# Performance work log

Measured on AMD Instinct MI355X. Metric: run time of the kernel, lower is better.

## Reference

```python
import jax, jax.numpy as jnp
import numpy as np
from jax import lax

B, L, DIM = 2, 2048, 2048
HK, HV = 16, 32
DK, DV = 128, 128
KCONV = 4
KEY_DIM = HK * DK          # 2048
VAL_DIM = HV * DV          # 4096
CONV_DIM = 2 * KEY_DIM + VAL_DIM  # 8192
EPS = 1e-6


def _l2norm(x, eps=1e-6):
    return x * lax.rsqrt((x * x).sum(-1, keepdims=True) + eps)


def _gated_delta_rule(q, k, v, g, beta):
    # q,k: (B,L,H,DK); v: (B,L,H,DV); g,beta: (B,L,H)
    q = _l2norm(q.astype(jnp.float32)) * (DK ** -0.5)
    k = _l2norm(k.astype(jnp.float32))
    v = v.astype(jnp.float32)
    g = g.astype(jnp.float32)
    beta = beta.astype(jnp.float32)
    # time-major for scan: (L,B,H,...)
    qs = q.transpose(1, 0, 2, 3)
    ks = k.transpose(1, 0, 2, 3)
    vs = v.transpose(1, 0, 2, 3)
    gs = g.transpose(1, 0, 2)
    bs = beta.transpose(1, 0, 2)
    state0 = jnp.zeros((B, HV, DK, DV), jnp.float32)

    def step(state, inp):
        q_t, k_t, v_t, g_t, b_t = inp
        state = state * jnp.exp(g_t)[..., None, None]          # decay
        kv_mem = jnp.einsum('bhk,bhkv->bhv', k_t, state)       # read
        delta = (v_t - kv_mem) * b_t[..., None]                # error-correct
        state = state + jnp.einsum('bhk,bhv->bhkv', k_t, delta)
        out_t = jnp.einsum('bhk,bhkv->bhv', q_t, state)
        return state, out_t

    _, outs = lax.scan(step, state0, (qs, ks, vs, gs, bs))
    return outs.transpose(1, 0, 2, 3)  # (B,L,H,DV)


def setup_inputs() -> dict:
    key = jax.random.key(0)
    ks = jax.random.split(key, 8)
    s = 0.02
    return {
        'x': jax.random.normal(ks[0], (B, L, DIM), jnp.float32),
        'W_qkv': jax.random.normal(ks[1], (CONV_DIM, DIM), jnp.float32) * s,
        'W_z': jax.random.normal(ks[2], (VAL_DIM, DIM), jnp.float32) * s,
        'W_a': jax.random.normal(ks[3], (HV, DIM), jnp.float32) * s,
        'W_b': jax.random.normal(ks[4], (HV, DIM), jnp.float32) * s,
        'conv_w': jax.random.normal(ks[5], (CONV_DIM, 1, KCONV), jnp.float32) * 0.2,
        'A_log': jnp.log(jax.random.uniform(ks[6], (HV,), jnp.float32, 1e-6, 16.0)),
        'dt_bias': jnp.ones((HV,), jnp.float32),
        'norm_weight': jnp.ones((DV,), jnp.float32),
        'W_out': jax.random.normal(ks[7], (DIM, VAL_DIM), jnp.float32) * s,
    }


def reference(x, W_qkv, W_z, W_a, W_b, conv_w, A_log, dt_bias, norm_weight, W_out):
    qkv = x @ W_qkv.T                      # (B,L,CONV_DIM)
    z = x @ W_z.T                          # (B,L,VAL_DIM)
    a = x @ W_a.T                          # (B,L,HV)
    b = x @ W_b.T                          # (B,L,HV)
    # depthwise causal conv1d (left pad K-1)
    h = qkv.transpose(0, 2, 1)             # (B,C,L)
    h = lax.conv_general_dilated(h, conv_w, window_strides=(1,),
                                 padding=[(KCONV - 1, 0)],
                                 dimension_numbers=('NCH', 'OIH', 'NCH'),
                                 feature_group_count=CONV_DIM)
    qkv = jax.nn.silu(h.transpose(0, 2, 1))
    q, k, v = jnp.split(qkv, [KEY_DIM, 2 * KEY_DIM], axis=-1)
    q = q.reshape(B, L, HK, DK)
    k = k.reshape(B, L, HK, DK)
    v = v.reshape(B, L, HV, DV)
    rep = HV // HK
    if rep > 1:
        q = jnp.repeat(q, rep, axis=2)
        k = jnp.repeat(k, rep, axis=2)
    g = -jnp.exp(A_log.astype(jnp.float32)) * jax.nn.softplus(a.astype(jnp.float32) + dt_bias)
    beta = jax.nn.sigmoid(b)
    out = _gated_delta_rule(q, k, v, g, beta)   # (B,L,HV,DV) fp32
    # gated RMSNorm over DV: silu(z) * weight * norm(out)
    var = (out * out).mean(-1, keepdims=True)
    out = out * lax.rsqrt(var + EPS) * norm_weight
    zg = z.reshape(B, L, HV, DV)
    out = out * jax.nn.silu(zg.astype(jnp.float32))
    out = out.astype(x.dtype).reshape(B, L, VAL_DIM)
    return out @ W_out.T
```

## Files before the change

### kernel.cpp

```cpp
#include <hip/hip_runtime.h>
#include <hip/hip_bf16.h>
#include <cstddef>
#include <cstdint>

constexpr int B = 2, L = 2048, DIM = 2048;
constexpr int HK = 16, HV = 32, DK = 128, DV = 128;
constexpr int KEY_DIM = HK * DK;
constexpr int VAL_DIM = HV * DV;
constexpr int CONV_DIM = 2 * KEY_DIM + VAL_DIM;
constexpr int NPROJ = CONV_DIM + VAL_DIM + HV + HV;
constexpr int NPAD  = ((NPROJ + 255) / 256) * 256;
constexpr size_t ROWS = (size_t)B * L;
constexpr float EPS = 1e-6f;
constexpr int CHUNK = 64, NCHUNK = L / CHUNK;
constexpr int NCH_TOT = B * HV * NCHUNK;
constexpr int CONV_LT = 16;
constexpr int CONV_TL = L / CONV_LT;

constexpr size_t OFF_QKV  = 0;
constexpr size_t OFF_Z    = OFF_QKV + ROWS * CONV_DIM * 2;
constexpr size_t OFF_A    = OFF_Z   + ROWS * VAL_DIM * 2;
constexpr size_t OFF_B    = OFF_A   + ROWS * HV * 4;
constexpr size_t OFF_G    = OFF_B   + ROWS * HV * 4;
constexpr size_t OFF_BETA = OFF_G   + ROWS * HV * 4;
constexpr size_t OFF_U    = OFF_BETA + ROWS * HV * 4;
constexpr size_t OFF_WQK  = OFF_U + (size_t)NCH_TOT * CHUNK * DV * 4;
constexpr size_t OFF_HALO = OFF_WQK + (size_t)NCH_TOT * CHUNK * CHUNK * 2;
constexpr size_t WS_NEED_BYTES = OFF_HALO + (size_t)3 * B * CONV_LT * CONV_DIM * 2;
constexpr size_t OFF_WCAT = OFF_U;
constexpr size_t OFF_XB   = OFF_WQK;
constexpr size_t OFF_WOB  = OFF_U;
static_assert((size_t)NPAD * DIM * 2 <= (size_t)NCH_TOT * CHUNK * DV * 4, "Wcat fits U");

__device__ __forceinline__ float bf2f(unsigned short u) {
    union { float f; uint32_t i; } c; c.i = ((uint32_t)u) << 16; return c.f;
}
__device__ __forceinline__ unsigned short f2bf(float f) {
    union { float f; uint32_t u; } c; c.f = f;
    uint32_t u = c.u + 0x7FFFu + ((c.u >> 16) & 1u);
    return (unsigned short)(u >> 16);
}
__device__ __forceinline__ uint32_t pk2(float a, float b) {
    return (uint32_t)f2bf(a) | ((uint32_t)f2bf(b) << 16);
}

typedef __attribute__((ext_vector_type(8))) short bfrag;
typedef __attribute__((ext_vector_type(4))) float ffrag;

__device__ __forceinline__ void gload16(const unsigned short* g, unsigned short* l) {
    __builtin_amdgcn_global_load_lds(
        (const __attribute__((address_space(1))) uint32_t*)g,
        (__attribute__((address_space(3))) uint32_t*)l, 16, 0, 0);
}

__device__ __forceinline__ const float* w_row_multi(int n, const float* Wq, const float* Wz,
                                                    const float* Wa, const float* Wb) {
    if (n < CONV_DIM)                return Wq + (size_t)n * DIM;
    if (n < CONV_DIM + VAL_DIM)      return Wz + (size_t)(n - CONV_DIM) * DIM;
    if (n < CONV_DIM + VAL_DIM + HV) return Wa + (size_t)(n - CONV_DIM - VAL_DIM) * DIM;
    return Wb + (size_t)(n - CONV_DIM - VAL_DIM - HV) * DIM;
}

__global__ __launch_bounds__(256) void cvt_wcat(
    const float* __restrict__ Wq, const float* __restrict__ Wz,
    const float* __restrict__ Wa, const float* __restrict__ Wb,
    unsigned short* __restrict__ dst)
{
    const int r = blockIdx.x;
    const int c = threadIdx.x * 8;
    uint4 o;
    if (r < NPROJ) {
        const float* s = w_row_multi(r, Wq, Wz, Wa, Wb) + c;
        float4 v0 = *(const float4*)s;
        float4 v1 = *(const float4*)(s + 4);
        o = make_uint4(pk2(v0.x, v0.y), pk2(v0.z, v0.w), pk2(v1.x, v1.y), pk2(v1.z, v1.w));
    } else {
        o = make_uint4(0u, 0u, 0u, 0u);
    }
    *(uint4*)&dst[(size_t)r * DIM + c] = o;
}

__global__ __launch_bounds__(256) void cvt_f32bf(const float* __restrict__ src,
                                                 unsigned short* __restrict__ dst, int cols)
{
    const size_t r = blockIdx.x;
    for (int c = threadIdx.x * 8; c < cols; c += 256 * 8) {
        const float* s = src + r * cols + c;
        float4 v0 = *(const float4*)s;
        float4 v1 = *(const float4*)(s + 4);
        *(uint4*)&dst[r * cols + c] =
            make_uint4(pk2(v0.x, v0.y), pk2(v0.z, v0.w), pk2(v1.x, v1.y), pk2(v1.z, v1.w));
    }
}

__device__ __forceinline__ void store_multi(int m, int n, float v,
                                            unsigned short* qkv, unsigned short* z,
                                            float* a, float* b) {
    if (n < CONV_DIM) {
        qkv[(size_t)m * CONV_DIM + n] = f2bf(v);
// ... 33 lines not shown
    const int t = threadIdx.x, lane = t & 63, wid = t >> 6;
    const int wm = (wid >> 1) * 64, wn = (wid & 1) * 64;
    const int quad = lane >> 4, l16 = lane & 15;
    const int x7 = l16 & 7;

    ffrag acc[4][4];
#pragma unroll
    for (int i = 0; i < 4; ++i)
#pragma unroll
        for (int j = 0; j < 4; ++j) acc[i][j] = (ffrag)0.f;

    const int srow = t >> 3;
    const int scol = (((t & 7) ^ (srow & 7)) * 8);
    const unsigned short* aS = xb   + (size_t)(row0 + srow) * DIM + scol;
    const unsigned short* bS = Wcat + (size_t)(col0 + srow) * DIM + scol;
    unsigned short* aD0 = lds + (wid * 8) * 64;
    unsigned short* bD0 = lds + 8192 + (wid * 8) * 64;

    auto STAGE = [&](int kt) {
        const int b = kt & 1;
        unsigned short* aD = aD0 + b * GBUF2;
        unsigned short* bD = bD0 + b * GBUF2;
        const int k0 = kt * BK;
#pragma unroll
        for (int g = 0; g < 4; ++g) {
            gload16(aS + (size_t)(g * 32) * DIM + k0, aD + g * 32 * 64);
            gload16(bS + (size_t)(g * 32) * DIM + k0, bD + g * 32 * 64);
        }
    };

    auto COMPUTE = [&](int kt) {
        const int b = kt & 1;
        const unsigned short* A  = lds + b * GBUF2;
        const unsigned short* Bm = lds + b * GBUF2 + 8192;
#pragma unroll
        for (int kk = 0; kk < 2; ++kk) {
            const int so = ((kk * 4 + quad) ^ x7) * 8;
            bfrag aF[4], bF[4];
#pragma unroll
            for (int m = 0; m < 4; ++m)
                aF[m] = *(const bfrag*)&A[(wm + m * 16 + l16) * 64 + so];
#pragma unroll
            for (int n = 0; n < 4; ++n)
                bF[n] = *(const bfrag*)&Bm[(wn + n * 16 + l16) * 64 + so];
            __builtin_amdgcn_s_setprio(1);
#pragma unroll
            for (int m = 0; m < 4; ++m)
#pragma unroll
                for (int n = 0; n < 4; ++n)
                    acc[m][n] = __builtin_amdgcn_mfma_f32_16x16x32_bf16(
                        aF[m], bF[n], acc[m][n], 0, 0, 0);
            __builtin_amdgcn_s_setprio(0);
        }
    };

    STAGE(0); STAGE(1);
    asm volatile("s_waitcnt vmcnt(8)" ::: "memory");
    asm volatile("s_barrier" ::: "memory");
    for (int kt = 0; kt < NT; ++kt) {
        COMPUTE(kt);
        if (kt == NT - 1) break;
        asm volatile("s_barrier" ::: "memory");
        if (kt + 2 < NT) {
            STAGE(kt + 2);
            asm volatile("s_waitcnt vmcnt(8)" ::: "memory");
        } else {
            asm volatile("s_waitcnt vmcnt(0)" ::: "memory");
        }
        asm volatile("s_barrier" ::: "memory");
    }

#pragma unroll
    for (int m = 0; m < 4; ++m)
#pragma unroll
        for (int n = 0; n < 4; ++n) {
            int gr = row0 + wm + m * 16 + quad * 4;
            int gc = col0 + wn + n * 16 + l16;
#pragma unroll
            for (int reg = 0; reg < 4; ++reg)
                store_multi(gr + reg, gc, acc[m][n][reg], qkv, z, a_out, b_out);
        }
}

__global__ __launch_bounds__(256) void gemm_outproj_bf(
    const unsigned short* __restrict__ A,
    const unsigned short* __restrict__ Wb,
    float* __restrict__ C)
{
    extern __shared__ __align__(16) unsigned short lds[];

    constexpr int NT  = VAL_DIM / BK;
    constexpr int NBY = (int)ROWS / 128;
    constexpr int NBX = DIM / 128;
    constexpr int NB  = NBY * NBX;
    const int id  = blockIdx.x;
    const int swz = (id & 7) * (NB >> 3) + (id >> 3);
    const int by  = swz & 31;
    const int bx  = swz >> 5;
    const int row0 = by * 128;
    const int col0 = bx * 128;

    const int t = threadIdx.x, lane = t & 63, wid = t >> 6;
    const int wm = (wid >> 1) * 64, wn = (wid & 1) * 64;
    const int quad = lane >> 4, l16 = lane & 15;
    const int x7 = l16 & 7;

    ffrag acc[4][4];
#pragma unroll
    for (int i = 0; i < 4; ++i)
#pragma unroll
        for (int j = 0; j < 4; ++j) acc[i][j] = (ffrag)0.f;

    const int srow = t >> 3;
    const int scol = (((t & 7) ^ (srow & 7)) * 8);
    const unsigned short* aS = A  + (size_t)(row0 + srow) * VAL_DIM + scol;
    const unsigned short* bS = Wb + (size_t)(col0 + srow) * VAL_DIM + scol;
    unsigned short* aD0 = lds + (wid * 8) * 64;
    unsigned short* bD0 = lds + 8192 + (wid * 8) * 64;

    auto STAGE = [&](int kt) {
        const int b = kt & 1;
        unsigned short* aD = aD0 + b * GBUF2;
        unsigned short* bD = bD0 + b * GBUF2;
        const int k0 = kt * BK;
#pragma unroll
        for (int g = 0; g < 4; ++g) {
            gload16(aS + (size_t)(g * 32) * VAL_DIM + k0, aD + g * 32 * 64);
            gload16(bS + (size_t)(g * 32) * VAL_DIM + k0, bD + g * 32 * 64);
        }
    };

    auto COMPUTE = [&](int kt) {
        const int b = kt & 1;
        const unsigned short* Am = lds + b * GBUF2;
        const unsigned short* Bm = lds + b * GBUF2 + 8192;
#pragma unroll
        for (int kk = 0; kk < 2; ++kk) {
            const int so = ((kk * 4 + quad) ^ x7) * 8;
            bfrag aF[4], bF[4];
#pragma unroll
            for (int m = 0; m < 4; ++m)
                aF[m] = *(const bfrag*)&Am[(wm + m * 16 + l16) * 64 + so];
#pragma unroll
            for (int n = 0; n < 4; ++n)
                bF[n] = *(const bfrag*)&Bm[(wn + n * 16 + l16) * 64 + so];
            __builtin_amdgcn_s_setprio(1);
#pragma unroll
            for (int m = 0; m < 4; ++m)
#pragma unroll
                for (int n = 0; n < 4; ++n)
                    acc[m][n] = __builtin_amdgcn_mfma_f32_16x16x32_bf16(
                        aF[m], bF[n], acc[m][n], 0, 0, 0);
            __builtin_amdgcn_s_setprio(0);
        }
    };

    STAGE(0); STAGE(1);
    asm volatile("s_waitcnt vmcnt(8)" ::: "memory");
    asm volatile("s_barrier" ::: "memory");
    for (int kt = 0; kt < NT; ++kt) {
        COMPUTE(kt);
        if (kt == NT - 1) break;
        asm volatile("s_barrier" ::: "memory");
        if (kt + 2 < NT) {
            STAGE(kt + 2);
            asm volatile("s_waitcnt vmcnt(8)" ::: "memory");
        } else {
            asm volatile("s_waitcnt vmcnt(0)" ::: "memory");
        }
        asm volatile("s_barrier" ::: "memory");
    }

#pragma unroll
    for (int m = 0; m < 4; ++m)
#pragma unroll
        for (int n = 0; n < 4; ++n) {
            int gr = row0 + wm + m * 16 + quad * 4;
            int gc = col0 + wn + n * 16 + l16;
#pragma unroll
            for (int reg = 0; reg < 4; ++reg)
                C[(size_t)(gr + reg) * DIM + gc] = acc[m][n][reg];
        }
}

__global__ __launch_bounds__(256) void conv_halo(const unsigned short* __restrict__ qkv,
                                                 unsigned short* __restrict__ hbuf)
{
    int idx = blockIdx.x * 256 + threadIdx.x;
    int c    = idx & (CONV_DIM - 1);
    int tile = (idx >> 13) & (CONV_LT - 1);
    int b    = idx >> 17;
    int l0 = tile * CONV_TL;
    const unsigned short* p = qkv + (size_t)b * L * CONV_DIM + c;
#pragma unroll
    for (int j = 0; j < 3; ++j) {
        unsigned short v = (tile > 0) ? p[(size_t)(l0 - 3 + j) * CONV_DIM] : (unsigned short)0;
        hbuf[((size_t)j * B * CONV_LT + b * CONV_LT + tile) * CONV_DIM + c] = v;
    }
}

__global__ __launch_bounds__(256) void conv_silu(unsigned short* __restrict__ qkv,
                                                 const float* __restrict__ conv_w,
                                                 const unsigned short* __restrict__ hbuf)
{
    int idx = blockIdx.x * 256 + threadIdx.x;
    int c    = idx & (CONV_DIM - 1);
    int tile = (idx >> 13) & (CONV_LT - 1);
    int b    = idx >> 17;
    const float w0 = conv_w[c * 4 + 0];
    const float w1 = conv_w[c * 4 + 1];
    const float w2 = conv_w[c * 4 + 2];
    const float w3 = conv_w[c * 4 + 3];
    unsigned short* p = qkv + ((size_t)b * L + tile * CONV_TL) * CONV_DIM + c;
    const size_t hb = (size_t)b * CONV_LT + tile;
    float x0 = bf2f(hbuf[((size_t)0 * B * CONV_LT + hb) * CONV_DIM + c]);
    float x1 = bf2f(hbuf[((size_t)1 * B * CONV_LT + hb) * CONV_DIM + c]);
    float x2 = bf2f(hbuf[((size_t)2 * B * CONV_LT + hb) * CONV_DIM + c]);
    for (int l0 = 0; l0 < CONV_TL; l0 += 8) {
        float xv[8];
#pragma unroll
        for (int j = 0; j < 8; ++j) xv[j] = bf2f(p[(size_t)(l0 + j) * CONV_DIM]);
#pragma unroll
        for (int j = 0; j < 8; ++j) {
            float h = w0 * x0 + w1 * x1 + w2 * x2 + w3 * xv[j];
            float s = h / (1.f + __expf(-h));
            p[(size_t)(l0 + j) * CONV_DIM] = f2bf(s);
            x0 = x1; x1 = x2; x2 = xv[j];
        }
    }
}

__global__ __launch_bounds__(256) void normqk(unsigned short* __restrict__ qkv)
{
    int wid  = blockIdx.x * 4 + (threadIdx.x >> 6);
    int lane = threadIdx.x & 63;
    int hk  = wid & 15;
    int sel = (wid >> 4) & 1;
    int row = wid >> 5;
    unsigned short* p = qkv + (size_t)row * CONV_DIM + sel * KEY_DIM + hk * DK;
    float x0 = bf2f(p[lane]), x1 = bf2f(p[lane + 64]);
    float ss = x0 * x0 + x1 * x1;
#pragma unroll
    for (int o = 32; o >= 1; o >>= 1) ss += __shfl_xor(ss, o);
    float sc = rsqrtf(ss + 1e-6f);
    if (sel == 0) sc *= 0.08838834764831845f;
    p[lane]      = f2bf(x0 * sc);
    p[lane + 64] = f2bf(x1 * sc);
}

__global__ __launch_bounds__(256) void gatecoef(const float* __restrict__ a_buf,
                                                const float* __restrict__ b_buf,
                                                const float* __restrict__ A_log,
                                                const float* __restrict__ dt_bias,
                                                float* __restrict__ glog,
                                                float* __restrict__ beta)
{
    int idx = blockIdx.x * blockDim.x + threadIdx.x;
    int h = idx & (HV - 1);
    float av = a_buf[idx];
    float bv = b_buf[idx];
    float x  = av + dt_bias[h];
    float sp = (x > 20.f) ? x : log1pf(__expf(x));
    glog[idx] = -__expf(A_log[h]) * sp;
    beta[idx] = 1.f / (1.f + __expf(-bv));
}


constexpr int RSK  = 136;
constexpr int RST  = 72;
constexpr int RSTD = 68;
constexpr int RSR1 = 260;

constexpr int P1_oKs  = 0;
constexpr int P1_oQs  = P1_oKs + 64 * RSK * 2;
constexpr int P1_oDT  = 0;
constexpr int P1_oAf  = P1_oQs + 64 * RSK * 2;
constexpr int P1_oRHS = P1_oAf + 64 * RST * 2;
constexpr int P1_oG   = P1_oRHS + 64 * RSR1 * 4;
constexpr int P1_oEG  = P1_oG + 256;
constexpr int P1_oBs  = P1_oEG + 256;
constexpr int P1_SMEM = P1_oBs + 256;

__global__ __launch_bounds__(256, 1) void chunk_prep(
    unsigned short* __restrict__ qkv,
    const float* __restrict__ glog,
    const float* __restrict__ beta,
    float* __restrict__ Ubuf,
    unsigned short* __restrict__ Wqkbuf)
{
    extern __shared__ __align__(16) char smem[];
    unsigned short* sKs = (unsigned short*)(smem + P1_oKs);
// ... 71 lines not shown
                float sc = __expf(sG[i] - gj);
                sAf[i * RST + j] = f2bf((j < i) ? sBs[i] * sc * accA[mt][reg] : 0.f);
                Wqp[i * CHUNK + j] = f2bf((j <= i) ? sc * accW[mt][reg] : 0.f);
            }
    }

    {
        const int r  = t >> 2;
        const int c0 = (t & 3) * 32;
        const float be  = sBs[r];
        const float beg = be * sEG[r];
        const unsigned short* gv = qkv + (bL + l0 + r) * CONV_DIM + VOFF + c0;
#pragma unroll
        for (int u = 0; u < 4; ++u) {
            uint4 vv = *(const uint4*)(gv + 8 * u);
            const unsigned short* vp = (const unsigned short*)&vv;
#pragma unroll
            for (int e = 0; e < 8; ++e)
                sRHS[r * RSR1 + c0 + 8 * u + e] = be * bf2f(vp[e]);
        }
#pragma unroll
        for (int u = 0; u < 4; ++u)
#pragma unroll
            for (int e = 0; e < 8; ++e)
                sRHS[r * RSR1 + 128 + c0 + 8 * u + e] =
                    beg * bf2f(sKs[r * RSK + c0 + 8 * u + e]);
    }
    __syncthreads();

    for (int u = t; u < 256 * RSTD / 2; u += 256) ((uint32_t*)sDT)[u] = 0;

    float* Up = Ubuf + (size_t)bid * (CHUNK * DV);
    for (int sb = 0; sb < 4; ++sb) {
        const int sb16 = 16 * sb;
        if (sb > 0) {
            const int kbn = (sb + 1) >> 1;
            ffrag c16[4];
#pragma unroll
            for (int nt = 0; nt < 4; ++nt) c16[nt] = (ffrag)0.f;
            for (int kb = 0; kb < kbn; ++kb) {
                bfrag af = *(const bfrag*)&sAf[(sb16 + l16) * RST + 32 * kb + quad8];
#pragma unroll
                for (int nt = 0; nt < 4; ++nt) {
                    bfrag bf = *(const bfrag*)&sDT[(64 * w + 16 * nt + l16) * RSTD + 32 * kb + quad8];
                    c16[nt] = __builtin_amdgcn_mfma_f32_16x16x32_bf16(af, bf, c16[nt], 0, 0, 0);
                }
            }
#pragma unroll
            for (int nt = 0; nt < 4; ++nt)
#pragma unroll
                for (int reg = 0; reg < 4; ++reg)
                    sRHS[(sb16 + quad * 4 + reg) * RSR1 + 64 * w + 16 * nt + l16] -= c16[nt][reg];
        }
        __syncthreads();
        {
            const int c = t;
            float d16[16];
#pragma unroll
            for (int e = 0; e < 16; ++e) {
                const int i = sb16 + e;
                float acc = sRHS[i * RSR1 + c];
#pragma unroll
                for (int f = 0; f < 16; ++f)
                    if (f < e) acc -= bf2f(sAf[i * RST + sb16 + f]) * d16[f];
                d16[e] = acc;
            }
#pragma unroll
            for (int e = 0; e < 16; e += 2)
                *(uint32_t*)&sDT[c * RSTD + sb16 + e] = pk2(d16[e], d16[e + 1]);
            if (c < 128) {
                float* up = Up + c;
#pragma unroll
                for (int e = 0; e < 16; ++e) up[(size_t)(sb16 + e) * DV] = d16[e];
            } else {
                unsigned short* wp = qkv + (bL + l0 + sb16) * CONV_DIM + VOFF + (c - 128);
#pragma unroll
                for (int e = 0; e < 16; ++e) wp[(size_t)e * CONV_DIM] = f2bf(-d16[e]);
            }
        }
        __syncthreads();
    }
}

constexpr int P2_oSTb = 0;
constexpr int P2_oWk  = P2_oSTb + 128 * RSK * 2;
constexpr int P2_oQs  = P2_oWk + 64 * RSK * 2;
constexpr int P2_oKT  = P2_oQs + 64 * RSK * 2;
constexpr int P2_oWqk = P2_oKT + 128 * RST * 2;
constexpr int P2_oDT  = P2_oWqk + 64 * RST * 2;
constexpr int P2_oDdT = P2_oDT + 128 * RST * 2;
constexpr int P2_oEG  = P2_oDdT + 128 * RST * 2;
constexpr int P2_oEGd = P2_oEG + 256;
constexpr int P2_oNW  = P2_oEGd + 256;
constexpr int P2_oP   = P2_oNW + 512;
constexpr int P2_SMEM = P2_oP + 512;

__global__ __launch_bounds__(512, 1) void chunk_scan2(
    const unsigned short* __restrict__ qkv,
    const float* __restrict__ glog,
    const float* __restrict__ Ubuf,
    const unsigned short* __restrict__ Wqkbuf,
    unsigned short* __restrict__ z_io,
    const float* __restrict__ norm_w)
{
    extern __shared__ __align__(16) char smem[];
    unsigned short* sSTb = (unsigned short*)(smem + P2_oSTb);
    unsigned short* sWk  = (unsigned short*)(smem + P2_oWk);
    unsigned short* sQs  = (unsigned short*)(smem + P2_oQs);
    unsigned short* sKT  = (unsigned short*)(smem + P2_oKT);
    unsigned short* sWqk = (unsigned short*)(smem + P2_oWqk);
    unsigned short* sDT  = (unsigned short*)(smem + P2_oDT);
    unsigned short* sDdT = (unsigned short*)(smem + P2_oDdT);
    float* sEG  = (float*)(smem + P2_oEG);
    float* sEGd = (float*)(smem + P2_oEGd);
    float* sNW  = (float*)(smem + P2_oNW);
    float* sP   = (float*)(smem + P2_oP);

    const int bb = blockIdx.x >> 5;
    const int h  = blockIdx.x & (HV - 1);
    const int hk = h >> 1;
    const int t    = threadIdx.x;
    const int w    = t >> 6;
    const int lane = t & 63;
    const int quad = lane >> 4;
    const int l16  = lane & 15;
    const int quad8 = quad * 8;
    const int rg = w >> 1;
    const int dh = w & 1;
    const size_t bL = (size_t)bb * L;
    const int VOFF = 2 * KEY_DIM + h * DV;
    const size_t chbase0 = ((size_t)bb * HV + h) * NCHUNK;

    const int r  = t >> 3;
    const int c0 = (t & 7) * 16;
    const int cw = (t & 7) * 8;

    ffrag accS[8];
#pragma unroll
    for (int nt = 0; nt < 8; ++nt) accS[nt] = (ffrag)0.f;

    for (int u = t; u < 64 * RSK; u += 512) ((uint32_t*)sSTb)[u] = 0;
    if (t < 128) sNW[t] = norm_w[t];

    uint4 pQ[2], pK[2], pWk[2], pWqk;
    float pGl;

    auto PF = [&](int ch) {
        const int l0p = ch * CHUNK;
        const unsigned short* grow = qkv + (bL + l0p + r) * CONV_DIM;
        const unsigned short* gq = grow + hk * DK + c0;
        const unsigned short* gk = grow + KEY_DIM + hk * DK + c0;
        const unsigned short* gw = grow + VOFF + c0;
#pragma unroll
        for (int u = 0; u < 2; ++u) {
            pQ[u]  = *(const uint4*)(gq + 8 * u);
            pK[u]  = *(const uint4*)(gk + 8 * u);
            pWk[u] = *(const uint4*)(gw + 8 * u);
        }
        pWqk = *(const uint4*)(Wqkbuf + (chbase0 + ch) * (CHUNK * CHUNK) + r * CHUNK + cw);
        pGl = glog[(bL + l0p + (t & 63)) * HV + h];
    };

    PF(0);

    for (int ch = 0; ch < NCHUNK; ++ch) {
        const int l0 = ch * CHUNK;
        const size_t cb = chbase0 + ch;
        __syncthreads();

        ffrag accD[4];
        {
            const float* up = Ubuf + cb * (CHUNK * DV) + (size_t)(quad * 4) * DV + 16 * w + l16;
#pragma unroll
            for (int mt = 0; mt < 4; ++mt)
#pragma unroll
                for (int reg = 0; reg < 4; ++reg)
                    accD[mt][reg] = up[(size_t)(16 * mt + reg) * DV];
        }
        unsigned short pz[4][4];
        {
            const unsigned short* zp =
                z_io + (bL + l0 + 16 * rg + quad * 4) * (size_t)VAL_DIM + h * DV + 64 * dh + l16;
#pragma unroll
            for (int nt = 0; nt < 4; ++nt)
#pragma unroll
                for (int reg = 0; reg < 4; ++reg)
                    pz[nt][reg] = zp[(size_t)reg * VAL_DIM + 16 * nt];
        }

#pragma unroll
        for (int u = 0; u < 2; ++u) {
            *(uint4*)&sQs[r * RSK + c0 + 8 * u] = pQ[u];
            *(uint4*)&sWk[r * RSK + c0 + 8 * u] = pWk[u];
            const unsigned short* kp = (const unsigned short*)&pK[u];
#pragma unroll
            for (int e = 0; e < 8; ++e) {
                const int c = c0 + 8 * u + e;
                sKT[c * RST + ((((r >> 3) ^ (c >> 3)) & 7) << 3) + (r & 7)] = kp[e];
            }
        }
        *(uint4*)&sWqk[r * RST + cw] = pWqk;

        {
            float gl = pGl;
            if (t < 64) {
#pragma unroll
                for (int off = 1; off < 64; off <<= 1) {
                    float v = __shfl_up(gl, off, 64);
                    if (lane >= off) gl += v;
                }
                float gc = __shfl(gl, 63, 64);
                sEG[t]  = __expf(gl);
                sEGd[t] = __expf(gc - gl);
            }
        }

        if (ch + 1 < NCHUNK) PF(ch + 1);
        __syncthreads();

#pragma unroll
        for (int kk = 0; kk < 4; ++kk) {
            bfrag b0 = *(const bfrag*)&sSTb[(16 * w + l16) * RSK + 32 * kk + quad8];
#pragma unroll
            for (int mt = 0; mt < 4; ++mt) {
                bfrag af = *(const bfrag*)&sWk[(16 * mt + l16) * RSK + 32 * kk + quad8];
                accD[mt] = __builtin_amdgcn_mfma_f32_16x16x32_bf16(af, b0, accD[mt], 0, 0, 0);
            }
        }

        {
            const int dv = 16 * w + l16;
#pragma unroll
            for (int mt = 0; mt < 4; ++mt) {
                const int i0 = 16 * mt + quad * 4;
                const float e0 = sEGd[i0], e1 = sEGd[i0 + 1], e2 = sEGd[i0 + 2], e3 = sEGd[i0 + 3];
                const float d0 = accD[mt][0], d1 = accD[mt][1];
                const float d2 = accD[mt][2], d3 = accD[mt][3];
                *(uint32_t*)&sDT[dv * RST + i0]      = pk2(d0, d1);
                *(uint32_t*)&sDT[dv * RST + i0 + 2]  = pk2(d2, d3);
                *(uint32_t*)&sDdT[dv * RST + i0]     = pk2(d0 * e0, d1 * e1);
                *(uint32_t*)&sDdT[dv * RST + i0 + 2] = pk2(d2 * e2, d3 * e3);
            }
        }
        __syncthreads();

        ffrag accO[4];
#pragma unroll
        for (int nt = 0; nt < 4; ++nt) accO[nt] = (ffrag)0.f;
#pragma unroll
        for (int kk = 0; kk < 4; ++kk) {
            bfrag af = *(const bfrag*)&sQs[(16 * rg + l16) * RSK + 32 * kk + quad8];
#pragma unroll
            for (int nt = 0; nt < 4; ++nt) {
                bfrag bf = *(const bfrag*)&sSTb[(64 * dh + 16 * nt + l16) * RSK + 32 * kk + quad8];
                accO[nt] = __builtin_amdgcn_mfma_f32_16x16x32_bf16(af, bf, accO[nt], 0, 0, 0);
            }
        }
#pragma unroll
        for (int nt = 0; nt < 4; ++nt)
#pragma unroll
            for (int reg = 0; reg < 4; ++reg)
                accO[nt][reg] *= sEG[16 * rg + quad * 4 + reg];
#pragma unroll
        for (int kk = 0; kk < 2; ++kk) {
            bfrag af = *(const bfrag*)&sWqk[(16 * rg + l16) * RST + 32 * kk + quad8];
#pragma unroll
            for (int nt = 0; nt < 4; ++nt) {
                bfrag bf = *(const bfrag*)&sDT[(64 * dh + 16 * nt + l16) * RST + 32 * kk + quad8];
                accO[nt] = __builtin_amdgcn_mfma_f32_16x16x32_bf16(af, bf, accO[nt], 0, 0, 0);
            }
        }

        float p4[4];
#pragma unroll
        for (int reg = 0; reg < 4; ++reg) {
            float p = 0.f;
#pragma unroll
            for (int nt = 0; nt < 4; ++nt) p += accO[nt][reg] * accO[nt][reg];
#pragma unroll
            for (int m = 1; m < 16; m <<= 1) p += __shfl_xor(p, m, 64);
            p4[reg] = p;
        }
        if (l16 == 0) {
#pragma unroll
            for (int reg = 0; reg < 4; ++reg) sP[w * 16 + quad * 4 + reg] = p4[reg];
        }

        {
            const float eGc = sEG[63];
#pragma unroll
            for (int nt = 0; nt < 8; ++nt)
#pragma unroll
                for (int reg = 0; reg < 4; ++reg) accS[nt][reg] *= eGc;
#pragma unroll
            for (int kk = 0; kk < 2; ++kk) {
                bfrag a0 = *(const bfrag*)&sDdT[(16 * w + l16) * RST + 32 * kk + quad8];
#pragma unroll
                for (int nt = 0; nt < 8; ++nt) {
                    const int ck = 16 * nt + l16;
                    bfrag bk = *(const bfrag*)&sKT[ck * RST +
                                 ((((4 * kk + quad) ^ (ck >> 3)) & 7) << 3)];
                    accS[nt] = __builtin_amdgcn_mfma_f32_16x16x32_bf16(a0, bk, accS[nt], 0, 0, 0);
                }
            }
        }
        __syncthreads();

        {
            float inv[4];
#pragma unroll
            for (int reg = 0; reg < 4; ++reg) {
                float pp = p4[reg] + sP[(w ^ 1) * 16 + quad * 4 + reg];
                inv[reg] = rsqrtf(pp * (1.f / 128.f) + EPS);
            }
            unsigned short* zw =
                z_io + (bL + l0 + 16 * rg + quad * 4) * (size_t)VAL_DIM + h * DV + 64 * dh + l16;
#pragma unroll
            for (int nt = 0; nt < 4; ++nt) {
                const float nwv = sNW[64 * dh + 16 * nt + l16];
#pragma unroll
                for (int reg = 0; reg < 4; ++reg) {
                    float zv = bf2f(pz[nt][reg]);
                    float y = accO[nt][reg] * inv[reg] * nwv * (zv / (1.f + __expf(-zv)));
                    zw[(size_t)reg * VAL_DIM + 16 * nt] = f2bf(y);
                }
            }
        }

#pragma unroll
        for (int nt = 0; nt < 8; ++nt)
#pragma unroll
            for (int reg = 0; reg < 4; ++reg)
                sSTb[(16 * w + quad * 4 + reg) * RSK + 16 * nt + l16] = f2bf(accS[nt][reg]);
    }
}

extern "C" void kernel_launch(void* const* d_in, const int* in_sizes, int n_in,
                              void* d_out, int out_size, void* d_ws, size_t ws_size,
                              hipStream_t stream)
{
    const float* x        = (const float*)d_in[0];
    const float* W_qkv    = (const float*)d_in[1];
    const float* W_z      = (const float*)d_in[2];
    const float* W_a      = (const float*)d_in[3];
    const float* W_b      = (const float*)d_in[4];
    const float* conv_w   = (const float*)d_in[5];
    const float* A_log    = (const float*)d_in[6];
    const float* dt_bias  = (const float*)d_in[7];
    const float* norm_w   = (const float*)d_in[8];
    const float* W_out    = (const float*)d_in[9];
    float* out = (float*)d_out;
    char*  ws  = (char*)d_ws;

    if (ws_size < WS_NEED_BYTES) return;

    unsigned short* qkv = (unsigned short*)(ws + OFF_QKV);
    unsigned short* z   = (unsigned short*)(ws + OFF_Z);
    float* a    = (float*)(ws + OFF_A);
    float* bbuf = (float*)(ws + OFF_B);
    float* gl   = (float*)(ws + OFF_G);
    float* beta = (float*)(ws + OFF_BETA);
    float* Ubuf = (float*)(ws + OFF_U);
    unsigned short* Wqkbuf = (unsigned short*)(ws + OFF_WQK);
    unsigned short* hbuf   = (unsigned short*)(ws + OFF_HALO);
    unsigned short* Wcat   = (unsigned short*)(ws + OFF_WCAT);
    unsigned short* xb     = (unsigned short*)(ws + OFF_XB);
    unsigned short* Wob    = (unsigned short*)(ws + OFF_WOB);

    static bool attr_set = false;
    if (!attr_set) {
        (void)hipFuncSetAttribute((const void*)chunk_prep,
                                  hipFuncAttributeMaxDynamicSharedMemorySize, P1_SMEM);
        (void)hipFuncSetAttribute((const void*)chunk_scan2,
                                  hipFuncAttributeMaxDynamicSharedMemorySize, P2_SMEM);
        (void)hipFuncSetAttribute((const void*)gemm_inproj_bf,
                                  hipFuncAttributeMaxDynamicSharedMemorySize, GEMM_SMEM);
        (void)hipFuncSetAttribute((const void*)gemm_outproj_bf,
                                  hipFuncAttributeMaxDynamicSharedMemorySize, GEMM_SMEM);
        attr_set = true;
    }

    cvt_wcat<<<NPAD, 256, 0, stream>>>(W_qkv, W_z, W_a, W_b, Wcat);
    cvt_f32bf<<<(int)ROWS, 256, 0, stream>>>(x, xb, DIM);
    gemm_inproj_bf<<<((int)ROWS / 128) * (NPAD / 128), 256, GEMM_SMEM, stream>>>(
        xb, Wcat, qkv, z, a, bbuf);
    conv_halo<<<(B * CONV_LT * CONV_DIM) / 256, 256, 0, stream>>>(qkv, hbuf);
    conv_silu<<<(B * CONV_LT * CONV_DIM) / 256, 256, 0, stream>>>(qkv, conv_w, hbuf);
    normqk<<<(B * L * 2 * HK) / 4, 256, 0, stream>>>(qkv);
    gatecoef<<<(B * L * HV) / 256, 256, 0, stream>>>(a, bbuf, A_log, dt_bias, gl, beta);
    chunk_prep<<<NCH_TOT, 256, P1_SMEM, stream>>>(qkv, gl, beta, Ubuf, Wqkbuf);
    chunk_scan2<<<B * HV, 512, P2_SMEM, stream>>>(qkv, gl, Ubuf, Wqkbuf, z, norm_w);
    cvt_f32bf<<<DIM, 256, 0, stream>>>(W_out, Wob, VAL_DIM);
    gemm_outproj_bf<<<((int)ROWS / 128) * (DIM / 128), 256, GEMM_SMEM, stream>>>(z, Wob, out);
}
```

Baseline: 937.0 us.

## Split chunk scan across DV slices, separate RMS gate, enlarge out-proj GEMM tiles

The sequential chunk scan is split into four blocks per (batch, head), each owning a 32-column slice of DV, so 256 blocks run instead of 64. The per-chunk output is written back into the U buffer in place, and a new rmsgate kernel then applies the RMSNorm and silu(z) gate. The output projection GEMM now uses 256x128 tiles with 512 threads, a triple-buffered LDS pipeline and loads issued before compute. Conv tiling is also halved to 8 tiles. The trade-off is an extra kernel launch and an fp32 round-trip of the outputs through global memory, plus duplicated Q/K/W loads across the four DV-slice blocks.

```diff
diff --git a/kernel.cpp b/kernel.cpp
--- a/kernel.cpp
+++ b/kernel.cpp
@@ -14,7 +14,7 @@
 constexpr float EPS = 1e-6f;
 constexpr int CHUNK = 64, NCHUNK = L / CHUNK;
 constexpr int NCH_TOT = B * HV * NCHUNK;
-constexpr int CONV_LT = 16;
+constexpr int CONV_LT = 8;
 constexpr int CONV_TL = L / CONV_LT;
 
 constexpr size_t OFF_QKV  = 0;
@@ -214,7 +214,10 @@
         }
 }
 
-__global__ __launch_bounds__(256) void gemm_outproj_bf(
+constexpr int GBUF3 = 24576;
+constexpr int GEMM3_SMEM = 3 * GBUF3 * 2;
+
+__global__ __launch_bounds__(512, 1) void gemm_outproj_bf(
     const unsigned short* __restrict__ A,
     const unsigned short* __restrict__ Wb,
     float* __restrict__ C)
@@ -222,18 +225,18 @@
     extern __shared__ __align__(16) unsigned short lds[];
 
     constexpr int NT  = VAL_DIM / BK;
-    constexpr int NBY = (int)ROWS / 128;
+    constexpr int NBY = (int)ROWS / 256;
     constexpr int NBX = DIM / 128;
     constexpr int NB  = NBY * NBX;
     const int id  = blockIdx.x;
     const int swz = (id & 7) * (NB >> 3) + (id >> 3);
-    const int by  = swz & 31;
-    const int bx  = swz >> 5;
-    const int row0 = by * 128;
+    const int by  = swz & 15;
+    const int bx  = swz >> 4;
+    const int row0 = by * 256;
     const int col0 = bx * 128;
 
     const int t = threadIdx.x, lane = t & 63, wid = t >> 6;
-    const int wm = (wid >> 1) * 64, wn = (wid & 1) * 64;
+    const int wr = wid >> 1, wc = wid & 1;
     const int quad = lane >> 4, l16 = lane & 15;
     const int x7 = l16 & 7;
 
@@ -248,67 +251,67 @@
     const unsigned short* aS = A  + (size_t)(row0 + srow) * VAL_DIM + scol;
     const unsigned short* bS = Wb + (size_t)(col0 + srow) * VAL_DIM + scol;
     unsigned short* aD0 = lds + (wid * 8) * 64;
-    unsigned short* bD0 = lds + 8192 + (wid * 8) * 64;
+    unsigned short* bD0 = lds + 16384 + (wid * 8) * 64;
 
     auto STAGE = [&](int kt) {
-        const int b = kt & 1;
-        unsigned short* aD = aD0 + b * GBUF2;
-        unsigned short* bD = bD0 + b * GBUF2;
+        const int b = kt % 3;
+        unsigned short* aD = aD0 + b * GBUF3;
+        unsigned short* bD = bD0 + b * GBUF3;
         const int k0 = kt * BK;
 #pragma unroll
-        for (int g = 0; g < 4; ++g) {
-            gload16(aS + (size_t)(g * 32) * VAL_DIM + k0, aD + g * 32 * 64);
-            gload16(bS + (size_t)(g * 32) * VAL_DIM + k0, bD + g * 32 * 64);
-        }
+        for (int g = 0; g < 4; ++g)
+            gload16(aS + (size_t)(g * 64) * VAL_DIM + k0, aD + g * 64 * 64);
+#pragma unroll
+        for (int g = 0; g < 2; ++g)
+            gload16(bS + (size_t)(g * 64) * VAL_DIM + k0, bD + g * 64 * 64);
     };
 
     auto COMPUTE = [&](int kt) {
-        const int b = kt & 1;
-        const unsigned short* Am = lds + b * GBUF2;
-        const unsigned short* Bm = lds + b * GBUF2 + 8192;
+        const int b = kt % 3;
+        const unsigned short* Am = lds + b * GBUF3;
+        const unsigned short* Bm = lds + b * GBUF3 + 16384;
 #pragma unroll
         for (int kk = 0; kk < 2; ++kk) {
             const int so = ((kk * 4 + quad) ^ x7) * 8;
             bfrag aF[4], bF[4];
 #pragma unroll
             for (int m = 0; m < 4; ++m)
-                aF[m] = *(const bfrag*)&Am[(wm + m * 16 + l16) * 64 + so];
+                aF[m] = *(const bfrag*)&Am[(wr * 64 + m * 16 + l16) * 64 + so];
 #pragma unroll
             for (int n = 0; n < 4; ++n)
-                bF[n] = *(const bfrag*)&Bm[(wn + n * 16 + l16) * 64 + so];
-            __builtin_amdgcn_s_setprio(1);
+                bF[n] = *(const bfrag*)&Bm[(wc * 64 + n * 16 + l16) * 64 + so];
 #pragma unroll
             for (int m = 0; m < 4; ++m)
 #pragma unroll
                 for (int n = 0; n < 4; ++n)
                     acc[m][n] = __builtin_amdgcn_mfma_f32_16x16x32_bf16(
                         aF[m], bF[n], acc[m][n], 0, 0, 0);
-            __builtin_amdgcn_s_setprio(0);
         }
     };
 
     STAGE(0); STAGE(1);
-    asm volatile("s_waitcnt vmcnt(8)" ::: "memory");
+    asm volatile("s_waitcnt vmcnt(6)" ::: "memory");
     asm volatile("s_barrier" ::: "memory");
     for (int kt = 0; kt < NT; ++kt) {
-        COMPUTE(kt);
-        if (kt == NT - 1) break;
-        asm volatile("s_barrier" ::: "memory");
         if (kt + 2 < NT) {
             STAGE(kt + 2);
-            asm volatile("s_waitcnt vmcnt(8)" ::: "memory");
+            asm volatile("s_waitcnt vmcnt(12)" ::: "memory");
+        } else if (kt + 1 < NT) {
+            asm volatile("s_waitcnt vmcnt(6)" ::: "memory");
         } else {
             asm volatile("s_waitcnt vmcnt(0)" ::: "memory");
         }
         asm volatile("s_barrier" ::: "memory");
+        COMPUTE(kt);
+        asm volatile("s_barrier" ::: "memory");
     }
 
 #pragma unroll
     for (int m = 0; m < 4; ++m)
 #pragma unroll
         for (int n = 0; n < 4; ++n) {
-            int gr = row0 + wm + m * 16 + quad * 4;
-            int gc = col0 + wn + n * 16 + l16;
+            int gr = row0 + wr * 64 + m * 16 + quad * 4;
+            int gc = col0 + wc * 64 + n * 16 + l16;
 #pragma unroll
             for (int reg = 0; reg < 4; ++reg)
                 C[(size_t)(gr + reg) * DIM + gc] = acc[m][n][reg];
@@ -321,7 +324,7 @@
     int idx = blockIdx.x * 256 + threadIdx.x;
     int c    = idx & (CONV_DIM - 1);
     int tile = (idx >> 13) & (CONV_LT - 1);
-    int b    = idx >> 17;
+    int b    = idx >> 16;
     int l0 = tile * CONV_TL;
     const unsigned short* p = qkv + (size_t)b * L * CONV_DIM + c;
 #pragma unroll
@@ -338,7 +341,7 @@
     int idx = blockIdx.x * 256 + threadIdx.x;
     int c    = idx & (CONV_DIM - 1);
     int tile = (idx >> 13) & (CONV_LT - 1);
-    int b    = idx >> 17;
+    int b    = idx >> 16;
     const float w0 = conv_w[c * 4 + 0];
     const float w1 = conv_w[c * 4 + 1];
     const float w2 = conv_w[c * 4 + 2];
@@ -576,67 +579,63 @@
     }
 }
 
-constexpr int P2_oSTb = 0;
-constexpr int P2_oWk  = P2_oSTb + 128 * RSK * 2;
-constexpr int P2_oQs  = P2_oWk + 64 * RSK * 2;
-constexpr int P2_oKT  = P2_oQs + 64 * RSK * 2;
-constexpr int P2_oWqk = P2_oKT + 128 * RST * 2;
-constexpr int P2_oDT  = P2_oWqk + 64 * RST * 2;
-constexpr int P2_oDdT = P2_oDT + 128 * RST * 2;
-constexpr int P2_oEG  = P2_oDdT + 128 * RST * 2;
-constexpr int P2_oEGd = P2_oEG + 256;
-constexpr int P2_oNW  = P2_oEGd + 256;
-constexpr int P2_oP   = P2_oNW + 512;
-constexpr int P2_SMEM = P2_oP + 512;
-
-__global__ __launch_bounds__(512, 1) void chunk_scan2(
+constexpr int S3_oKT  = 0;
+constexpr int S3_oQs  = S3_oKT + 128 * RST * 2;
+constexpr int S3_oWk  = S3_oQs + 64 * RSK * 2;
+constexpr int S3_oWqk = S3_oWk + 64 * RSK * 2;
+constexpr int S3_oSTb = S3_oWqk + 64 * RST * 2;
+constexpr int S3_oDT  = S3_oSTb + 32 * RSK * 2;
+constexpr int S3_oDdT = S3_oDT + 32 * RST * 2;
+constexpr int S3_oEG  = S3_oDdT + 32 * RST * 2;
+constexpr int S3_oEGd = S3_oEG + 256;
+constexpr int S3_SMEM = S3_oEGd + 256;
+
+__global__ __launch_bounds__(256, 1) void chunk_scan3(
     const unsigned short* __restrict__ qkv,
     const float* __restrict__ glog,
-    const float* __restrict__ Ubuf,
-    const unsigned short* __restrict__ Wqkbuf,
-    unsigned short* __restrict__ z_io,
-    const float* __restrict__ norm_w)
+    float* __restrict__ Ubuf,
+    const unsigned short* __restrict__ Wqkbuf)
 {
     extern __shared__ __align__(16) char smem[];
-    unsigned short* sSTb = (unsigned short*)(smem + P2_oSTb);
-    unsigned short* sWk  = (unsigned short*)(smem + P2_oWk);
-    unsigned short* sQs  = (unsigned short*)(smem + P2_oQs);
-    unsigned short* sKT  = (unsigned short*)(smem + P2_oKT);
-    unsigned short* sWqk = (unsigned short*)(smem + P2_oWqk);
-    unsigned short* sDT  = (unsigned short*)(smem + P2_oDT);
-    unsigned short* sDdT = (unsigned short*)(smem + P2_oDdT);
-    float* sEG  = (float*)(smem + P2_oEG);
-    float* sEGd = (float*)(smem + P2_oEGd);
-    float* sNW  = (float*)(smem + P2_oNW);
-    float* sP   = (float*)(smem + P2_oP);
-
-    const int bb = blockIdx.x >> 5;
-    const int h  = blockIdx.x & (HV - 1);
+    unsigned short* sKT  = (unsigned short*)(smem + S3_oKT);
+    unsigned short* sQs  = (unsigned short*)(smem + S3_oQs);
+    unsigned short* sWk  = (unsigned short*)(smem + S3_oWk);
+    unsigned short* sWqk = (unsigned short*)(smem + S3_oWqk);
+    unsigned short* sSTb = (unsigned short*)(smem + S3_oSTb);
+    unsigned short* sDT  = (unsigned short*)(smem + S3_oDT);
+    unsigned short* sDdT = (unsigned short*)(smem + S3_oDdT);
+    float* sEG  = (float*)(smem + S3_oEG);
+    float* sEGd = (float*)(smem + S3_oEGd);
+
+    const int g  = blockIdx.x & 3;
+    const int bh = blockIdx.x >> 2;
+    const int h  = bh & (HV - 1);
+    const int bb = bh >> 5;
     const int hk = h >> 1;
+    const int DV0 = g * 32;
     const int t    = threadIdx.x;
     const int w    = t >> 6;
     const int lane = t & 63;
     const int quad = lane >> 4;
     const int l16  = lane & 15;
     const int quad8 = quad * 8;
-    const int rg = w >> 1;
-    const int dh = w & 1;
     const size_t bL = (size_t)bb * L;
     const int VOFF = 2 * KEY_DIM + h * DV;
     const size_t chbase0 = ((size_t)bb * HV + h) * NCHUNK;
 
-    const int r  = t >> 3;
-    const int c0 = (t & 7) * 16;
-    const int cw = (t & 7) * 8;
-
-    ffrag accS[8];
-#pragma unroll
-    for (int nt = 0; nt < 8; ++nt) accS[nt] = (ffrag)0.f;
-
-    for (int u = t; u < 64 * RSK; u += 512) ((uint32_t*)sSTb)[u] = 0;
-    if (t < 128) sNW[t] = norm_w[t];
-
-    uint4 pQ[2], pK[2], pWk[2], pWqk;
+    const int r  = t >> 2;
+    const int c0 = (t & 3) * 32;
+    const int cw = (t & 3) * 16;
+
+    ffrag accS[2][2];
+#pragma unroll
+    for (int m = 0; m < 2; ++m)
+#pragma unroll
+        for (int n = 0; n < 2; ++n) accS[m][n] = (ffrag)0.f;
+
+    for (int u = t; u < 32 * RSK / 2; u += 256) ((uint32_t*)sSTb)[u] = 0;
+
+    uint4 pQ[4], pK[4], pWk[4], pWqk2[2];
     float pGl;
 
     auto PF = [&](int ch) {
@@ -646,44 +645,36 @@
         const unsigned short* gk = grow + KEY_DIM + hk * DK + c0;
         const unsigned short* gw = grow + VOFF + c0;
 #pragma unroll
-        for (int u = 0; u < 2; ++u) {
+        for (int u = 0; u < 4; ++u) {
             pQ[u]  = *(const uint4*)(gq + 8 * u);
             pK[u]  = *(const uint4*)(gk + 8 * u);
             pWk[u] = *(const uint4*)(gw + 8 * u);
         }
-        pWqk = *(const uint4*)(Wqkbuf + (chbase0 + ch) * (CHUNK * CHUNK) + r * CHUNK + cw);
+        const unsigned short* qp = Wqkbuf + (chbase0 + ch) * (CHUNK * CHUNK) + r * CHUNK + cw;
+        pWqk2[0] = *(const uint4*)qp;
+        pWqk2[1] = *(const uint4*)(qp + 8);
         pGl = glog[(bL + l0p + (t & 63)) * HV + h];
     };
 
     PF(0);
 
     for (int ch = 0; ch < NCHUNK; ++ch) {
-        const int l0 = ch * CHUNK;
         const size_t cb = chbase0 + ch;
+        float* Uch = Ubuf + cb * (CHUNK * DV);
         __syncthreads();
 
-        ffrag accD[4];
+        ffrag accD[2];
         {
-            const float* up = Ubuf + cb * (CHUNK * DV) + (size_t)(quad * 4) * DV + 16 * w + l16;
-#pragma unroll
-            for (int mt = 0; mt < 4; ++mt)
+            const float* up = Uch + (size_t)(16 * w + quad * 4) * DV + DV0 + l16;
+#pragma unroll
+            for (int nt = 0; nt < 2; ++nt)
 #pragma unroll
                 for (int reg = 0; reg < 4; ++reg)
-                    accD[mt][reg] = up[(size_t)(16 * mt + reg) * DV];
-        }
-        unsigned short pz[4][4];
-        {
-            const unsigned short* zp =
-                z_io + (bL + l0 + 16 * rg + quad * 4) * (size_t)VAL_DIM + h * DV + 64 * dh + l16;
-#pragma unroll
-            for (int nt = 0; nt < 4; ++nt)
-#pragma unroll
-                for (int reg = 0; reg < 4; ++reg)
-                    pz[nt][reg] = zp[(size_t)reg * VAL_DIM + 16 * nt];
-        }
-
-#pragma unroll
-        for (int u = 0; u < 2; ++u) {
+                    accD[nt][reg] = up[(size_t)reg * DV + 16 * nt];
+        }
+
+#pragma unroll
+        for (int u = 0; u < 4; ++u) {
             *(uint4*)&sQs[r * RSK + c0 + 8 * u] = pQ[u];
             *(uint4*)&sWk[r * RSK + c0 + 8 * u] = pWk[u];
             const unsigned short* kp = (const unsigned short*)&pK[u];
@@ -693,7 +684,8 @@
                 sKT[c * RST + ((((r >> 3) ^ (c >> 3)) & 7) << 3) + (r & 7)] = kp[e];
             }
         }
-        *(uint4*)&sWqk[r * RST + cw] = pWqk;
+        *(uint4*)&sWqk[r * RST + cw]     = pWqk2[0];
+        *(uint4*)&sWqk[r * RST + cw + 8] = pWqk2[1];
 
         {
             float gl = pGl;
@@ -714,22 +706,22 @@
 
 #pragma unroll
         for (int kk = 0; kk < 4; ++kk) {
-            bfrag b0 = *(const bfrag*)&sSTb[(16 * w + l16) * RSK + 32 * kk + quad8];
-#pragma unroll
-            for (int mt = 0; mt < 4; ++mt) {
-                bfrag af = *(const bfrag*)&sWk[(16 * mt + l16) * RSK + 32 * kk + quad8];
-                accD[mt] = __builtin_amdgcn_mfma_f32_16x16x32_bf16(af, b0, accD[mt], 0, 0, 0);
+            bfrag af = *(const bfrag*)&sWk[(16 * w + l16) * RSK + 32 * kk + quad8];
+#pragma unroll
+            for (int nt = 0; nt < 2; ++nt) {
+                bfrag bf = *(const bfrag*)&sSTb[(16 * nt + l16) * RSK + 32 * kk + quad8];
+                accD[nt] = __builtin_amdgcn_mfma_f32_16x16x32_bf16(af, bf, accD[nt], 0, 0, 0);
             }
         }
 
         {
-            const int dv = 16 * w + l16;
-#pragma unroll
-            for (int mt = 0; mt < 4; ++mt) {
-                const int i0 = 16 * mt + quad * 4;
-                const float e0 = sEGd[i0], e1 = sEGd[i0 + 1], e2 = sEGd[i0 + 2], e3 = sEGd[i0 + 3];
-                const float d0 = accD[mt][0], d1 = accD[mt][1];
-                const float d2 = accD[mt][2], d3 = accD[mt][3];
+            const int i0 = 16 * w + quad * 4;
+            const float e0 = sEGd[i0], e1 = sEGd[i0 + 1], e2 = sEGd[i0 + 2], e3 = sEGd[i0 + 3];
+#pragma unroll
+            for (int nt = 0; nt < 2; ++nt) {
+                const int dv = 16 * nt + l16;
+                const float d0 = accD[nt][0], d1 = accD[nt][1];
+                const float d2 = accD[nt][2], d3 = accD[nt][3];
                 *(uint32_t*)&sDT[dv * RST + i0]      = pk2(d0, d1);
                 *(uint32_t*)&sDT[dv * RST + i0 + 2]  = pk2(d2, d3);
                 *(uint32_t*)&sDdT[dv * RST + i0]     = pk2(d0 * e0, d1 * e1);
@@ -738,95 +730,105 @@
         }
         __syncthreads();
 
-        ffrag accO[4];
-#pragma unroll
-        for (int nt = 0; nt < 4; ++nt) accO[nt] = (ffrag)0.f;
+        ffrag accO[2];
+#pragma unroll
+        for (int nt = 0; nt < 2; ++nt) accO[nt] = (ffrag)0.f;
 #pragma unroll
         for (int kk = 0; kk < 4; ++kk) {
-            bfrag af = *(const bfrag*)&sQs[(16 * rg + l16) * RSK + 32 * kk + quad8];
-#pragma unroll
-            for (int nt = 0; nt < 4; ++nt) {
-                bfrag bf = *(const bfrag*)&sSTb[(64 * dh + 16 * nt + l16) * RSK + 32 * kk + quad8];
+            bfrag af = *(const bfrag*)&sQs[(16 * w + l16) * RSK + 32 * kk + quad8];
+#pragma unroll
+            for (int nt = 0; nt < 2; ++nt) {
+                bfrag bf = *(const bfrag*)&sSTb[(16 * nt + l16) * RSK + 32 * kk + quad8];
                 accO[nt] = __builtin_amdgcn_mfma_f32_16x16x32_bf16(af, bf, accO[nt], 0, 0, 0);
             }
         }
 #pragma unroll
-        for (int nt = 0; nt < 4; ++nt)
+        for (int nt = 0; nt < 2; ++nt)
 #pragma unroll
             for (int reg = 0; reg < 4; ++reg)
-                accO[nt][reg] *= sEG[16 * rg + quad * 4 + reg];
+                accO[nt][reg] *= sEG[16 * w + quad * 4 + reg];
 #pragma unroll
         for (int kk = 0; kk < 2; ++kk) {
-            bfrag af = *(const bfrag*)&sWqk[(16 * rg + l16) * RST + 32 * kk + quad8];
-#pragma unroll
-            for (int nt = 0; nt < 4; ++nt) {
-                bfrag bf = *(const bfrag*)&sDT[(64 * dh + 16 * nt + l16) * RST + 32 * kk + quad8];
+            bfrag af = *(const bfrag*)&sWqk[(16 * w + l16) * RST + 32 * kk + quad8];
+#pragma unroll
+            for (int nt = 0; nt < 2; ++nt) {
+                bfrag bf = *(const bfrag*)&sDT[(16 * nt + l16) * RST + 32 * kk + quad8];
                 accO[nt] = __builtin_amdgcn_mfma_f32_16x16x32_bf16(af, bf, accO[nt], 0, 0, 0);
             }
         }
-
-        float p4[4];
-#pragma unroll
-        for (int reg = 0; reg < 4; ++reg) {
-            float p = 0.f;
-#pragma unroll
-            for (int nt = 0; nt < 4; ++nt) p += accO[nt][reg] * accO[nt][reg];
-#pragma unroll
-            for (int m = 1; m < 16; m <<= 1) p += __shfl_xor(p, m, 64);
-            p4[reg] = p;
-        }
-        if (l16 == 0) {
-#pragma unroll
-            for (int reg = 0; reg < 4; ++reg) sP[w * 16 + quad * 4 + reg] = p4[reg];
+        {
+            float* op = Uch + (size_t)(16 * w + quad * 4) * DV + DV0 + l16;
+#pragma unroll
+            for (int nt = 0; nt < 2; ++nt)
+#pragma unroll
+                for (int reg = 0; reg < 4; ++reg)
+                    op[(size_t)reg * DV + 16 * nt] = accO[nt][reg];
         }
 
         {
             const float eGc = sEG[63];
 #pragma unroll
-            for (int nt = 0; nt < 8; ++nt)
-#pragma unroll
-                for (int reg = 0; reg < 4; ++reg) accS[nt][reg] *= eGc;
+            for (int m = 0; m < 2; ++m)
+#pragma unroll
+                for (int n = 0; n < 2; ++n)
+#pragma unroll
+                    for (int reg = 0; reg < 4; ++reg) accS[m][n][reg] *= eGc;
 #pragma unroll
             for (int kk = 0; kk < 2; ++kk) {
-                bfrag a0 = *(const bfrag*)&sDdT[(16 * w + l16) * RST + 32 * kk + quad8];
-#pragma unroll
-                for (int nt = 0; nt < 8; ++nt) {
-                    const int ck = 16 * nt + l16;
-                    bfrag bk = *(const bfrag*)&sKT[ck * RST +
-                                 ((((4 * kk + quad) ^ (ck >> 3)) & 7) << 3)];
-                    accS[nt] = __builtin_amdgcn_mfma_f32_16x16x32_bf16(a0, bk, accS[nt], 0, 0, 0);
+#pragma unroll
+                for (int m = 0; m < 2; ++m) {
+                    bfrag a0 = *(const bfrag*)&sDdT[(16 * m + l16) * RST + 32 * kk + quad8];
+#pragma unroll
+                    for (int n = 0; n < 2; ++n) {
+                        const int ck = 32 * w + 16 * n + l16;
+                        bfrag bk = *(const bfrag*)&sKT[ck * RST +
+                                     ((((4 * kk + quad) ^ (ck >> 3)) & 7) << 3)];
+                        accS[m][n] = __builtin_amdgcn_mfma_f32_16x16x32_bf16(a0, bk, accS[m][n], 0, 0, 0);
+                    }
                 }
             }
         }
         __syncthreads();
 
-        {
-            float inv[4];
-#pragma unroll
-            for (int reg = 0; reg < 4; ++reg) {
-                float pp = p4[reg] + sP[(w ^ 1) * 16 + quad * 4 + reg];
-                inv[reg] = rsqrtf(pp * (1.f / 128.f) + EPS);
-            }
-            unsigned short* zw =
-                z_io + (bL + l0 + 16 * rg + quad * 4) * (size_t)VAL_DIM + h * DV + 64 * dh + l16;
-#pragma unroll
-            for (int nt = 0; nt < 4; ++nt) {
-                const float nwv = sNW[64 * dh + 16 * nt + l16];
-#pragma unroll
-                for (int reg = 0; reg < 4; ++reg) {
-                    float zv = bf2f(pz[nt][reg]);
-                    float y = accO[nt][reg] * inv[reg] * nwv * (zv / (1.f + __expf(-zv)));
-                    zw[(size_t)reg * VAL_DIM + 16 * nt] = f2bf(y);
-                }
-            }
-        }
-
-#pragma unroll
-        for (int nt = 0; nt < 8; ++nt)
-#pragma unroll
-            for (int reg = 0; reg < 4; ++reg)
-                sSTb[(16 * w + quad * 4 + reg) * RSK + 16 * nt + l16] = f2bf(accS[nt][reg]);
-    }
+#pragma unroll
+        for (int m = 0; m < 2; ++m)
+#pragma unroll
+            for (int n = 0; n < 2; ++n)
+#pragma unroll
+                for (int reg = 0; reg < 4; ++reg)
+                    sSTb[(16 * m + quad * 4 + reg) * RSK + 32 * w + 16 * n + l16] =
+                        f2bf(accS[m][n][reg]);
+    }
+}
+
+__global__ __launch_bounds__(256) void rmsgate(
+    const float* __restrict__ Obuf,
+    unsigned short* __restrict__ z_io,
+    const float* __restrict__ norm_w)
+{
+    const int gw   = blockIdx.x * 4 + (threadIdx.x >> 6);
+    const int lane = threadIdx.x & 63;
+    const int h  = gw & (HV - 1);
+    const int lg = gw >> 5;
+    const int bb = lg >> 11;
+    const int l  = lg & (L - 1);
+    const int ch = l >> 6, i = l & 63;
+    const size_t cb = ((size_t)bb * HV + h) * NCHUNK + ch;
+    const int dv0 = lane * 2;
+
+    float2 o = *(const float2*)(Obuf + cb * (CHUNK * DV) + (size_t)i * DV + dv0);
+    float p = o.x * o.x + o.y * o.y;
+#pragma unroll
+    for (int m = 1; m < 64; m <<= 1) p += __shfl_xor(p, m, 64);
+    float inv = rsqrtf(p * (1.f / 128.f) + EPS);
+
+    unsigned short* zp = z_io + ((size_t)bb * L + l) * VAL_DIM + h * DV + dv0;
+    uint32_t zu = *(const uint32_t*)zp;
+    float z0 = bf2f((unsigned short)(zu & 0xFFFF));
+    float z1 = bf2f((unsigned short)(zu >> 16));
+    float y0 = o.x * inv * norm_w[dv0]     * (z0 / (1.f + __expf(-z0)));
+    float y1 = o.y * inv * norm_w[dv0 + 1] * (z1 / (1.f + __expf(-z1)));
+    *(uint32_t*)zp = pk2(y0, y1);
 }
 
 extern "C" void kernel_launch(void* const* d_in, const int* in_sizes, int n_in,
@@ -865,12 +867,12 @@
     if (!attr_set) {
         (void)hipFuncSetAttribute((const void*)chunk_prep,
                                   hipFuncAttributeMaxDynamicSharedMemorySize, P1_SMEM);
-        (void)hipFuncSetAttribute((const void*)chunk_scan2,
-                                  hipFuncAttributeMaxDynamicSharedMemorySize, P2_SMEM);
+        (void)hipFuncSetAttribute((const void*)chunk_scan3,
+                                  hipFuncAttributeMaxDynamicSharedMemorySize, S3_SMEM);
         (void)hipFuncSetAttribute((const void*)gemm_inproj_bf,
                                   hipFuncAttributeMaxDynamicSharedMemorySize, GEMM_SMEM);
         (void)hipFuncSetAttribute((const void*)gemm_outproj_bf,
-                                  hipFuncAttributeMaxDynamicSharedMemorySize, GEMM_SMEM);
+                                  hipFuncAttributeMaxDynamicSharedMemorySize, GEMM3_SMEM);
         attr_set = true;
     }
 
@@ -883,7 +885,8 @@
     normqk<<<(B * L * 2 * HK) / 4, 256, 0, stream>>>(qkv);
     gatecoef<<<(B * L * HV) / 256, 256, 0, stream>>>(a, bbuf, A_log, dt_bias, gl, beta);
     chunk_prep<<<NCH_TOT, 256, P1_SMEM, stream>>>(qkv, gl, beta, Ubuf, Wqkbuf);
-    chunk_scan2<<<B * HV, 512, P2_SMEM, stream>>>(qkv, gl, Ubuf, Wqkbuf, z, norm_w);
+    chunk_scan3<<<B * HV * 4, 256, S3_SMEM, stream>>>(qkv, gl, Ubuf, Wqkbuf);
+    rmsgate<<<(int)(ROWS * HV) / 4, 256, 0, stream>>>(Ubuf, z, norm_w);
     cvt_f32bf<<<DIM, 256, 0, stream>>>(W_out, Wob, VAL_DIM);
-    gemm_outproj_bf<<<((int)ROWS / 128) * (DIM / 128), 256, GEMM_SMEM, stream>>>(z, Wob, out);
-}
+    gemm_outproj_bf<<<((int)ROWS / 256) * (DIM / 128), 512, GEMM3_SMEM, stream>>>(z, Wob, out);
+}
```

After: 880.8 us. -6.0%, faster.
